# Performance work log

Hardware: AMD Instinct MI355X
Metric: run time of the kernel (lower is better)

## Reference

```python
import jax, jax.numpy as jnp
import numpy as np

N = 8192
IN_FEATS = 512
OUT_FEATS = 256
NEG_SLOPE = 0.01  # torch nn.LeakyReLU default


def setup_inputs() -> dict:
    key = jax.random.key(0)
    k_adj, k_feat, k_w, k_b, k_a1, k_a2 = jax.random.split(key, 6)
    adj_matrix = jax.random.uniform(k_adj, (N, N), dtype=jnp.float32)
    eye_matrix = jnp.eye(N, dtype=jnp.float32)  # identity adjacency, per AAGNN usage
    subgraph_feats = jax.random.normal(k_feat, (N, IN_FEATS), dtype=jnp.float32)
    node_mask = jnp.ones((N,), dtype=bool)
    # nn.Linear(in_feats, out_feats) params (kaiming-uniform-ish init scale)
    lim = 1.0 / np.sqrt(IN_FEATS)
    W = jax.random.uniform(k_w, (OUT_FEATS, IN_FEATS), minval=-lim, maxval=lim, dtype=jnp.float32)
    b = jax.random.uniform(k_b, (OUT_FEATS,), minval=-lim, maxval=lim, dtype=jnp.float32)
    # a_1, a_2 ~ torch.rand(1, out_feats)
    a_1 = jax.random.uniform(k_a1, (1, OUT_FEATS), dtype=jnp.float32)
    a_2 = jax.random.uniform(k_a2, (1, OUT_FEATS), dtype=jnp.float32)
    return {"adj_matrix": adj_matrix, "eye_matrix": eye_matrix,
            "subgraph_feats": subgraph_feats, "node_mask": node_mask,
            "W": W, "b": b, "a_1": a_1, "a_2": a_2}


def reference(adj_matrix, eye_matrix, subgraph_feats, node_mask, W, b, a_1, a_2):
    # z = Linear(subgraph_feats)  -> [N, out]
    z = subgraph_feats @ W.T + b
    zi = jnp.sum(a_1 * z, axis=1, keepdims=True)  # [N,1]
    zj = jnp.sum(a_2 * z, axis=1, keepdims=True)  # [N,1]
    # masked attention scores: adj*zi + adj*(eye*zj), leakyrelu, row softmax
    scores = jax.nn.leaky_relu(adj_matrix * zi + adj_matrix * (eye_matrix * zj),
                               negative_slope=NEG_SLOPE)
    att = jax.nn.softmax(scores, axis=1)  # [N,N]
    h = z - att @ z  # [N, out]
    out = jax.nn.relu(h)
    # original returns relu(h[node_mask]); mask is all-True -> same rows, static shape
    return jnp.where(node_mask[:, None], out, 0.0)
```

## Files before the change

### kernel.cpp

```cpp
#include <hip/hip_runtime.h>

#define N_NODES 8192
#define IN_F 512
#define OUT_F 256
#define KSPLIT 8
#define KCHUNK (N_NODES / KSPLIT)

typedef float f32x4 __attribute__((ext_vector_type(4)));
typedef short short8 __attribute__((ext_vector_type(8)));
typedef short short4v __attribute__((ext_vector_type(4)));

__device__ __forceinline__ unsigned short f2bf(float f) {
  unsigned int u = __float_as_uint(f);
  return (unsigned short)((u + 0x8000u) >> 16);
}

__device__ __forceinline__ short8 pack8(const float4& a, const float4& b) {
  short8 r;
  r[0] = (short)f2bf(a.x); r[1] = (short)f2bf(a.y);
  r[2] = (short)f2bf(a.z); r[3] = (short)f2bf(a.w);
  r[4] = (short)f2bf(b.x); r[5] = (short)f2bf(b.y);
  r[6] = (short)f2bf(b.z); r[7] = (short)f2bf(b.w);
  return r;
}

__global__ __launch_bounds__(256) void zgemm_mfma(
    const float* __restrict__ feats, const float* __restrict__ W,
    const float* __restrict__ bias, const float* __restrict__ a1v,
    const float* __restrict__ a2v, float* __restrict__ z,
    unsigned short* __restrict__ zF, float* __restrict__ zi_out,
    float* __restrict__ zj_out) {
  __shared__ float zred[4][32][2];
  const int tid = threadIdx.x;
  const int w = tid >> 6;
  const int l = tid & 63;
  const int g4 = l >> 4;
  const int gm = l & 15;
  const int ib = blockIdx.x * 32;

  f32x4 acc[2][4];
#pragma unroll
  for (int a = 0; a < 2; ++a)
#pragma unroll
    for (int b = 0; b < 4; ++b) acc[a][b] = (f32x4){0.f, 0.f, 0.f, 0.f};

#pragma unroll 2
  for (int ks = 0; ks < 16; ++ks) {
    const int k0 = ks * 32 + g4 * 8;
    short8 afr[2], bfr[4];
#pragma unroll
    for (int it = 0; it < 2; ++it) {
      const float* p = &feats[(size_t)(ib + it * 16 + gm) * IN_F + k0];
      afr[it] = pack8(*(const float4*)p, *(const float4*)(p + 4));
    }
#pragma unroll
    for (int nt = 0; nt < 4; ++nt) {
      const float* p = &W[(size_t)(w * 64 + nt * 16 + gm) * IN_F + k0];
      bfr[nt] = pack8(*(const float4*)p, *(const float4*)(p + 4));
    }
#pragma unroll
    for (int it = 0; it < 2; ++it)
#pragma unroll
      for (int nt = 0; nt < 4; ++nt)
        acc[it][nt] = __builtin_amdgcn_mfma_f32_16x16x32_bf16(
            afr[it], bfr[nt], acc[it][nt], 0, 0, 0);
  }

  const int kb = ib >> 5;
  float pzi[8] = {}, pzj[8] = {};
#pragma unroll
  for (int ntz = 0; ntz < 4; ++ntz) {
    const int col = w * 64 + ntz * 16 + gm;
    const float bv = bias[col];
    const float A1 = a1v[col], A2 = a2v[col];
    const int nt = w * 4 + ntz;
#pragma unroll
    for (int it = 0; it < 2; ++it) {
      short4v q;
#pragma unroll
      for (int r = 0; r < 4; ++r) {
        const int row = ib + it * 16 + g4 * 4 + r;
        const float v = acc[it][ntz][r] + bv;
        z[(size_t)row * OUT_F + col] = v;
        q[r] = (short)f2bf(v);
        pzi[it * 4 + r] += A1 * v;
        pzj[it * 4 + r] += A2 * v;
      }
      const int lane = (it * 2 + (g4 >> 1)) * 16 + gm;
      const int eb = (g4 & 1) * 4;
      *(short4v*)&zF[(size_t)(nt * 256 + kb) * 512 + lane * 8 + eb] = q;
    }
  }
#pragma unroll
  for (int off = 1; off < 16; off <<= 1)
#pragma unroll
    for (int q = 0; q < 8; ++q) {
      pzi[q] += __shfl_xor(pzi[q], off);
      pzj[q] += __shfl_xor(pzj[q], off);
    }
  if (gm == 0) {
#pragma unroll
    for (int it = 0; it < 2; ++it)
#pragma unroll
      for (int r = 0; r < 4; ++r) {
        zred[w][it * 16 + g4 * 4 + r][0] = pzi[it * 4 + r];
        zred[w][it * 16 + g4 * 4 + r][1] = pzj[it * 4 + r];
      }
  }
  __syncthreads();
  if (tid < 64) {
    const int row = tid >> 1, which = tid & 1;
    const float s = zred[0][row][which] + zred[1][row][which] +
                    zred[2][row][which] + zred[3][row][which];
    if (which == 0) zi_out[ib + row] = s;
    else zj_out[ib + row] = s;
  }
}

__global__ __launch_bounds__(256) void p_kernel(
    const float* __restrict__ adj, const float* __restrict__ zi_in,
    const float* __restrict__ zj_in, unsigned short* __restrict__ Pn) {
  __shared__ float red[4];
  const int row = blockIdx.x;
  const int tid = threadIdx.x;
  const float zir = zi_in[row];
  const float zjr = zj_in[row];
  const float* rp = adj + (size_t)row * N_NODES + tid * 4;

  f32x4 a[8];
#pragma unroll
  for (int c = 0; c < 8; ++c)
    a[c] = __builtin_nontemporal_load((const f32x4*)(rp + c * 1024));

  float p[32];
  float psum = 0.f;
#pragma unroll
  for (int c = 0; c < 8; ++c)
#pragma unroll
    for (int e = 0; e < 4; ++e) {
      const int j = c * 1024 + tid * 4 + e;
      const float av = a[c][e];
      float s = av * zir;
      if (j == row) s += av * zjr;
      s = fmaxf(s, 0.01f * s);
      const float pe = __expf(s);
      p[c * 4 + e] = pe;
      psum += pe;
    }
#pragma unroll
  for (int i = 0; i < 32; ++i) asm volatile("" : "+v"(p[i]));

#pragma unroll
  for (int off = 32; off > 0; off >>= 1) psum += __shfl_xor(psum, off);
  if ((tid & 63) == 0) red[tid >> 6] = psum;
  __syncthreads();
  const float rinv = 1.f / (red[0] + red[1] + red[2] + red[3]);

  unsigned short* op = Pn + (size_t)row * N_NODES + tid * 4;
#pragma unroll
  for (int c = 0; c < 8; ++c) {
    short4v v;
#pragma unroll
    for (int e = 0; e < 4; ++e) v[e] = (short)f2bf(p[c * 4 + e] * rinv);
    *(short4v*)(op + c * 1024) = v;
  }
}

__global__ __launch_bounds__(256, 3) void pz_gemm(
    const unsigned short* __restrict__ Pn,
    const unsigned short* __restrict__ zF, float* __restrict__ acc_ws) {
  __shared__ __align__(16) unsigned short Pt[2][64][64];
  const int tid = threadIdx.x;
  const int w = tid >> 6;
  const int l = tid & 63;
  const int l4 = l >> 4;
  const int lm = l & 15;
  const int mt = blockIdx.x & 127;
  const int kc = blockIdx.x >> 7;
  const int ib = mt * 64;
  const int jb0 = kc * KCHUNK;

  f32x4 acc[4][4];
#pragma unroll
  for (int a = 0; a < 4; ++a)
#pragma unroll
    for (int b = 0; b < 4; ++b) acc[a][b] = (f32x4){0.f, 0.f, 0.f, 0.f};

  const int NST = KCHUNK / 64;

#pragma unroll
  for (int m = 0; m < 2; ++m) {
    const int g = m * 256 + tid, r = g >> 3, s = g & 7;
    *(short8*)&Pt[0][r][(s ^ (r & 7)) * 8] =
        *(const short8*)&Pn[(size_t)(ib + r) * N_NODES + jb0 + s * 8];
  }

  for (int st = 0; st < NST; ++st) {
    const int b = st & 1;
    __syncthreads();

    short8 pg[2];
    if (st + 1 < NST) {
      const int jb = jb0 + (st + 1) * 64;
#pragma unroll
      for (int m = 0; m < 2; ++m) {
        const int g = m * 256 + tid, r = g >> 3, s = g & 7;
        pg[m] = *(const short8*)&Pn[(size_t)(ib + r) * N_NODES + jb + s * 8];
      }
    }

    const int kb0 = (jb0 + st * 64) >> 5;
    short8 bfr[2][4];
#pragma unroll
    for (int kk = 0; kk < 2; ++kk)
#pragma unroll
      for (int ntz = 0; ntz < 4; ++ntz)
        bfr[kk][ntz] = *(const short8*)&zF[(size_t)((w * 4 + ntz) * 256 +
                                                    kb0 + kk) * 512 + l * 8];

#pragma unroll
    for (int it = 0; it < 4; ++it) {
      const int r = it * 16 + lm;
#pragma unroll
      for (int kk = 0; kk < 2; ++kk) {
        const short8 afr =
            *(const short8*)&Pt[b][r][((kk * 4 + l4) ^ (r & 7)) * 8];
#pragma unroll
        for (int ntz = 0; ntz < 4; ++ntz)
          acc[it][ntz] = __builtin_amdgcn_mfma_f32_16x16x32_bf16(
              afr, bfr[kk][ntz], acc[it][ntz], 0, 0, 0);
      }
    }

    __syncthreads();

    if (st + 1 < NST) {
#pragma unroll
      for (int m = 0; m < 2; ++m) {
        const int g = m * 256 + tid, r = g >> 3, s = g & 7;
        *(short8*)&Pt[b ^ 1][r][(s ^ (r & 7)) * 8] = pg[m];
      }
    }
  }

#pragma unroll
  for (int it = 0; it < 4; ++it)
#pragma unroll
    for (int nt = 0; nt < 4; ++nt)
#pragma unroll
      for (int r = 0; r < 4; ++r) {
        const int gi = ib + it * 16 + l4 * 4 + r;
        const int gn = w * 64 + nt * 16 + lm;
        acc_ws[((size_t)kc * N_NODES + gi) * OUT_F + gn] = acc[it][nt][r];
      }
}

__global__ void finalize_kernel(const float* __restrict__ z,
                                const float* __restrict__ acc_ws,
                                float* __restrict__ out) {
  const int i = blockIdx.x;
  const int n = threadIdx.x;
  float a = 0.f;
#pragma unroll
  for (int kc = 0; kc < KSPLIT; ++kc)
    a += acc_ws[((size_t)kc * N_NODES + i) * OUT_F + n];
  const float v = z[(size_t)i * OUT_F + n] - a;
  out[(size_t)i * OUT_F + n] = fmaxf(v, 0.f);
}

extern "C" void kernel_launch(void* const* d_in, const int* in_sizes, int n_in,
                              void* d_out, int out_size, void* d_ws,
                              size_t ws_size, hipStream_t stream) {
  (void)in_sizes; (void)n_in; (void)out_size; (void)ws_size;
  const float* adj = (const float*)d_in[0];
  const float* feats = (const float*)d_in[2];
  const float* W = (const float*)d_in[4];
  const float* bias = (const float*)d_in[5];
  const float* a1v = (const float*)d_in[6];
  const float* a2v = (const float*)d_in[7];
  float* out = (float*)d_out;

  char* ws = (char*)d_ws;
  float* z = (float*)ws;
  unsigned short* zF = (unsigned short*)(ws + ((size_t)8 << 20));
  float* zi = (float*)(ws + ((size_t)12 << 20));
  float* zj = zi + N_NODES;
  float* acc_ws = (float*)(ws + ((size_t)16 << 20));
  unsigned short* Pn = (unsigned short*)(ws + ((size_t)96 << 20));

  hipLaunchKernelGGL(zgemm_mfma, dim3(N_NODES / 32), dim3(256), 0, stream,
                     feats, W, bias, a1v, a2v, z, zF, zi, zj);
  hipLaunchKernelGGL(p_kernel, dim3(N_NODES), dim3(256), 0, stream, adj, zi,
                     zj, Pn);
  hipLaunchKernelGGL(pz_gemm, dim3(128 * KSPLIT), dim3(256), 0, stream, Pn,
                     zF, acc_ws);
  hipLaunchKernelGGL(finalize_kernel, dim3(N_NODES), dim3(256), 0, stream, z,
                     acc_ws, out);
}
```

Before: 148.1 us.

## Defer softmax normalization to finalize and retile PZ GEMM to 32-row tiles

The p_kernel now writes unnormalized bf16 exponentials in a single pass and stores the row sum to a workspace, instead of keeping 32 values live in registers until the reduction finishes. Dividing by the row sum moves to finalize_kernel, after the split-K accumulation. The P·Z GEMM changes from 64-row tiles with 8-way K split to 32-row tiles with 4-way K split. That halves the partial-sum workspace traffic and gives smaller per-block accumulator state, at the cost of less reuse of each Z fragment load per block.

```diff
diff --git a/kernel.cpp b/kernel.cpp
--- a/kernel.cpp
+++ b/kernel.cpp
@@ -3,7 +3,7 @@
 #define N_NODES 8192
 #define IN_F 512
 #define OUT_F 256
-#define KSPLIT 8
+#define KSPLIT 4
 #define KCHUNK (N_NODES / KSPLIT)
 
 typedef float f32x4 __attribute__((ext_vector_type(4)));
@@ -13,6 +13,10 @@
 __device__ __forceinline__ unsigned short f2bf(float f) {
   unsigned int u = __float_as_uint(f);
   return (unsigned short)((u + 0x8000u) >> 16);
+}
+
+__device__ __forceinline__ float bf2f(unsigned short b) {
+  return __uint_as_float(((unsigned int)b) << 16);
 }
 
 __device__ __forceinline__ short8 pack8(const float4& a, const float4& b) {
@@ -119,7 +123,8 @@
 
 __global__ __launch_bounds__(256) void p_kernel(
     const float* __restrict__ adj, const float* __restrict__ zi_in,
-    const float* __restrict__ zj_in, unsigned short* __restrict__ Pn) {
+    const float* __restrict__ zj_in, unsigned short* __restrict__ Pn,
+    float* __restrict__ l_ws) {
   __shared__ float red[4];
   const int row = blockIdx.x;
   const int tid = threadIdx.x;
@@ -132,10 +137,11 @@
   for (int c = 0; c < 8; ++c)
     a[c] = __builtin_nontemporal_load((const f32x4*)(rp + c * 1024));
 
-  float p[32];
   float psum = 0.f;
-#pragma unroll
-  for (int c = 0; c < 8; ++c)
+  unsigned short* op = Pn + (size_t)row * N_NODES + tid * 4;
+#pragma unroll
+  for (int c = 0; c < 8; ++c) {
+    short4v v;
 #pragma unroll
     for (int e = 0; e < 4; ++e) {
       const int j = c * 1024 + tid * 4 + e;
@@ -143,71 +149,56 @@
       float s = av * zir;
       if (j == row) s += av * zjr;
       s = fmaxf(s, 0.01f * s);
-      const float pe = __expf(s);
-      p[c * 4 + e] = pe;
-      psum += pe;
-    }
-#pragma unroll
-  for (int i = 0; i < 32; ++i) asm volatile("" : "+v"(p[i]));
+      const unsigned short pb = f2bf(__expf(s));
+      psum += bf2f(pb);
+      v[e] = (short)pb;
+    }
+    *(short4v*)(op + c * 1024) = v;
+  }
 
 #pragma unroll
   for (int off = 32; off > 0; off >>= 1) psum += __shfl_xor(psum, off);
   if ((tid & 63) == 0) red[tid >> 6] = psum;
   __syncthreads();
-  const float rinv = 1.f / (red[0] + red[1] + red[2] + red[3]);
-
-  unsigned short* op = Pn + (size_t)row * N_NODES + tid * 4;
-#pragma unroll
-  for (int c = 0; c < 8; ++c) {
-    short4v v;
-#pragma unroll
-    for (int e = 0; e < 4; ++e) v[e] = (short)f2bf(p[c * 4 + e] * rinv);
-    *(short4v*)(op + c * 1024) = v;
-  }
+  if (tid == 0) l_ws[row] = red[0] + red[1] + red[2] + red[3];
 }
 
 __global__ __launch_bounds__(256, 3) void pz_gemm(
     const unsigned short* __restrict__ Pn,
     const unsigned short* __restrict__ zF, float* __restrict__ acc_ws) {
-  __shared__ __align__(16) unsigned short Pt[2][64][64];
+  __shared__ __align__(16) unsigned short Pt[2][32][64];
   const int tid = threadIdx.x;
   const int w = tid >> 6;
   const int l = tid & 63;
   const int l4 = l >> 4;
   const int lm = l & 15;
-  const int mt = blockIdx.x & 127;
-  const int kc = blockIdx.x >> 7;
-  const int ib = mt * 64;
+  const int mt = blockIdx.x & 255;
+  const int kc = blockIdx.x >> 8;
+  const int ib = mt * 32;
   const int jb0 = kc * KCHUNK;
 
-  f32x4 acc[4][4];
-#pragma unroll
-  for (int a = 0; a < 4; ++a)
+  const int sr = tid >> 3;
+  const int ss = tid & 7;
+
+  f32x4 acc[2][4];
+#pragma unroll
+  for (int a = 0; a < 2; ++a)
 #pragma unroll
     for (int b = 0; b < 4; ++b) acc[a][b] = (f32x4){0.f, 0.f, 0.f, 0.f};
 
   const int NST = KCHUNK / 64;
 
-#pragma unroll
-  for (int m = 0; m < 2; ++m) {
-    const int g = m * 256 + tid, r = g >> 3, s = g & 7;
-    *(short8*)&Pt[0][r][(s ^ (r & 7)) * 8] =
-        *(const short8*)&Pn[(size_t)(ib + r) * N_NODES + jb0 + s * 8];
-  }
+  *(short8*)&Pt[0][sr][(ss ^ (sr & 7)) * 8] =
+      *(const short8*)&Pn[(size_t)(ib + sr) * N_NODES + jb0 + ss * 8];
 
   for (int st = 0; st < NST; ++st) {
     const int b = st & 1;
     __syncthreads();
 
-    short8 pg[2];
-    if (st + 1 < NST) {
-      const int jb = jb0 + (st + 1) * 64;
-#pragma unroll
-      for (int m = 0; m < 2; ++m) {
-        const int g = m * 256 + tid, r = g >> 3, s = g & 7;
-        pg[m] = *(const short8*)&Pn[(size_t)(ib + r) * N_NODES + jb + s * 8];
-      }
-    }
+    short8 pg;
+    if (st + 1 < NST)
+      pg = *(const short8*)&Pn[(size_t)(ib + sr) * N_NODES + jb0 +
+                               (st + 1) * 64 + ss * 8];
 
     const int kb0 = (jb0 + st * 64) >> 5;
     short8 bfr[2][4];
@@ -219,7 +210,7 @@
                                                     kb0 + kk) * 512 + l * 8];
 
 #pragma unroll
-    for (int it = 0; it < 4; ++it) {
+    for (int it = 0; it < 2; ++it) {
       const int r = it * 16 + lm;
 #pragma unroll
       for (int kk = 0; kk < 2; ++kk) {
@@ -234,17 +225,12 @@
 
     __syncthreads();
 
-    if (st + 1 < NST) {
-#pragma unroll
-      for (int m = 0; m < 2; ++m) {
-        const int g = m * 256 + tid, r = g >> 3, s = g & 7;
-        *(short8*)&Pt[b ^ 1][r][(s ^ (r & 7)) * 8] = pg[m];
-      }
-    }
-  }
-
-#pragma unroll
-  for (int it = 0; it < 4; ++it)
+    if (st + 1 < NST)
+      *(short8*)&Pt[b ^ 1][sr][(ss ^ (sr & 7)) * 8] = pg;
+  }
+
+#pragma unroll
+  for (int it = 0; it < 2; ++it)
 #pragma unroll
     for (int nt = 0; nt < 4; ++nt)
 #pragma unroll
@@ -257,14 +243,16 @@
 
 __global__ void finalize_kernel(const float* __restrict__ z,
                                 const float* __restrict__ acc_ws,
+                                const float* __restrict__ l_ws,
                                 float* __restrict__ out) {
   const int i = blockIdx.x;
   const int n = threadIdx.x;
+  const float ls = l_ws[i];
   float a = 0.f;
 #pragma unroll
   for (int kc = 0; kc < KSPLIT; ++kc)
     a += acc_ws[((size_t)kc * N_NODES + i) * OUT_F + n];
-  const float v = z[(size_t)i * OUT_F + n] - a;
+  const float v = z[(size_t)i * OUT_F + n] - a / ls;
   out[(size_t)i * OUT_F + n] = fmaxf(v, 0.f);
 }
 
@@ -285,15 +273,16 @@
   unsigned short* zF = (unsigned short*)(ws + ((size_t)8 << 20));
   float* zi = (float*)(ws + ((size_t)12 << 20));
   float* zj = zi + N_NODES;
+  float* l_ws = (float*)(ws + ((size_t)13 << 20));
   float* acc_ws = (float*)(ws + ((size_t)16 << 20));
   unsigned short* Pn = (unsigned short*)(ws + ((size_t)96 << 20));
 
   hipLaunchKernelGGL(zgemm_mfma, dim3(N_NODES / 32), dim3(256), 0, stream,
                      feats, W, bias, a1v, a2v, z, zF, zi, zj);
   hipLaunchKernelGGL(p_kernel, dim3(N_NODES), dim3(256), 0, stream, adj, zi,
-                     zj, Pn);
-  hipLaunchKernelGGL(pz_gemm, dim3(128 * KSPLIT), dim3(256), 0, stream, Pn,
+                     zj, Pn, l_ws);
+  hipLaunchKernelGGL(pz_gemm, dim3(256 * KSPLIT), dim3(256), 0, stream, Pn,
                      zF, acc_ws);
   hipLaunchKernelGGL(finalize_kernel, dim3(N_NODES), dim3(256), 0, stream, z,
-                     acc_ws, out);
-}
+                     acc_ws, l_ws, out);
+}
```

Measured after the change: 157.8 us. 1.07x slower.
